# Kernel optimization log

Hardware: AMD Instinct MI355X
Metric: run time of the kernel (lower is better)

Reference implementation:

```python
import jax, jax.numpy as jnp
import numpy as np

OUT, IN = 8192, 8192
GROUP = 128
N_GROUPS = IN // GROUP
BATCH = 64


def dequant_int4(packed, scales):
    # packed: [OUT, IN//2] int32 bytes in [0,256); two 4-bit codes per byte
    low = packed & 0xF            # first element of each pair
    high = (packed >> 4) & 0xF    # second element
    q = jnp.stack([low, high], axis=-1).reshape(OUT, IN)  # interleaved nibbles
    # symmetric grouped dequant: w = (q - 8) * scale, scale per [row, group]
    qg = q.reshape(OUT, N_GROUPS, GROUP).astype(scales.dtype)
    w = (qg - 8.0) * scales[:, :, None]
    return w.reshape(OUT, IN)


def setup_inputs() -> dict:
    key = jax.random.key(0)
    k1, k2, k3 = jax.random.split(key, 3)
    x = jax.random.normal(k1, (BATCH, IN), dtype=jnp.float32)
    packed = jax.random.randint(k2, (OUT, IN // 2), 0, 256, dtype=jnp.int32)
    scales = jax.random.uniform(k3, (OUT, N_GROUPS), dtype=jnp.float32)
    return {"x": x, "packed": packed, "scales": scales}


def reference(x, packed, scales):
    # Dequantize int4 weights then dense matmul (F.linear, no bias)
    w = dequant_int4(packed, scales)        # [OUT, IN]
    return jnp.einsum('bi,oi->bo', x, w)    # [BATCH, OUT]
```

## Files before the change

kernel.cpp:

```cpp
#include <hip/hip_runtime.h>
#include <hip/hip_bf16.h>
#include <stdint.h>

#define OUTN   8192
#define INN    8192
#define NGRP   64
#define BATCHN 64
#define KSPLIT 8
#define KCHUNK (INN / KSPLIT)
#define NITER  (KCHUNK / 128)
#define OSZ    (BATCHN * OUTN)

typedef __attribute__((ext_vector_type(8))) short bf16x8;
typedef __attribute__((ext_vector_type(4))) float f32x4;
typedef __attribute__((ext_vector_type(4))) unsigned int u32x4;

__device__ __forceinline__ unsigned short f2bf(float f) {
  __hip_bfloat16 h = __float2bfloat16(f);
  return __builtin_bit_cast(unsigned short, h);
}
__device__ __forceinline__ float bf2f(unsigned short h) {
  unsigned int u = ((unsigned int)h) << 16;
  return __builtin_bit_cast(float, u);
}

__global__ void qlin_prep(const float* __restrict__ x, float* __restrict__ xsum) {
  const int b = blockIdx.x;
  const int t = threadIdx.x;
  const float* xrow = x + (size_t)b * INN + t * 32;
  float s = 0.0f;
#pragma unroll
  for (int i = 0; i < 8; ++i) {
    float4 v = *(const float4*)(xrow + i * 4);
    s += bf2f(f2bf(v.x)) + bf2f(f2bf(v.y)) + bf2f(f2bf(v.z)) + bf2f(f2bf(v.w));
  }
  __shared__ float part[256];
  part[t] = s;
  __syncthreads();
  if (t < NGRP) {
    float g = part[4 * t] + part[4 * t + 1] + part[4 * t + 2] + part[4 * t + 3];
    xsum[t * BATCHN + b] = g;
  }
}

__global__ void qlin_swz(const float* __restrict__ x, unsigned short* __restrict__ xswz) {
  const int idx = blockIdx.x * 256 + threadIdx.x;
  const int b  = idx & 63;
  const int kb = idx >> 6;
  const float* p = x + (size_t)b * INN + kb * 8;
  float4 v0 = *(const float4*)p;
  float4 v1 = *(const float4*)(p + 4);
  u32x4 o;
  o.x = (unsigned)f2bf(v0.x) | ((unsigned)f2bf(v0.y) << 16);
  o.y = (unsigned)f2bf(v0.z) | ((unsigned)f2bf(v0.w) << 16);
  o.z = (unsigned)f2bf(v1.x) | ((unsigned)f2bf(v1.y) << 16);
  o.w = (unsigned)f2bf(v1.z) | ((unsigned)f2bf(v1.w) << 16);
  *(u32x4*)&xswz[(size_t)idx * 8] = o;
}

__global__ __launch_bounds__(256, 4) void qlin_main(
    const int* __restrict__ packed, const float* __restrict__ scales,
    const unsigned short* __restrict__ xswz, const float* __restrict__ xsum,
    float* __restrict__ out, float* __restrict__ part) {
  const int bx    = blockIdx.x;
  const int ks    = bx & (KSPLIT - 1);
  const int ntile = bx >> 3;
  const int o0    = ntile * 64;
  const int g0    = ks * NITER;

  const int t    = threadIdx.x;
  const int lane = t & 63;
  const int w    = t >> 6;
  const int r    = lane & 15;
  const int q    = lane >> 4;
  const int orow = o0 + w * 16 + r;

  __shared__ float xs[NITER][BATCHN];
#pragma unroll
  for (int i = 0; i < 2; ++i) {
    int v = t * 2 + i;
    xs[v >> 6][v & 63] = xsum[(g0 + (v >> 6)) * BATCHN + (v & 63)];
  }

  float4 sa = *(const float4*)&scales[(size_t)orow * NGRP + g0];
  float4 sb = *(const float4*)&scales[(size_t)orow * NGRP + g0 + 4];
  float sreg[8] = {sa.x, sa.y, sa.z, sa.w, sb.x, sb.y, sb.z, sb.w};

  const int* bptr = packed + (size_t)orow * (INN / 2) + ks * (KCHUNK / 2) + q * 4;
  const unsigned short* aptr = xswz + ((size_t)(ks * 128 + q) * 64 + r) * 8;

  __syncthreads();

  f32x4 facc[4];
#pragma unroll
  for (int mt = 0; mt < 4; ++mt) facc[mt] = (f32x4){0.f, 0.f, 0.f, 0.f};

  int4 b4[4], b4n[4];
#pragma unroll
  for (int kq = 0; kq < 4; ++kq) b4[kq] = *(const int4*)(bptr + kq * 16);

  for (int i = 0; i < NITER; ++i) {
    f32x4 gacc[4];
#pragma unroll
    for (int mt = 0; mt < 4; ++mt) gacc[mt] = (f32x4){0.f, 0.f, 0.f, 0.f};

#pragma unroll
    for (int kq = 0; kq < 4; ++kq) {
      bf16x8 af[4];
#pragma unroll
      for (int mt = 0; mt < 4; ++mt)
        af[mt] = *(const bf16x8*)(aptr + ((size_t)(i * 16 + kq * 4) * 64 + mt * 16) * 8);

      int4 c = b4[kq];
      u32x4 bw0, bw1;
      bw0.x = 0x43004300u | ((unsigned)c.x & 0xFu) | (((unsigned)c.x & 0xF0u) << 12);
      bw0.y = 0x43004300u | ((unsigned)c.y & 0xFu) | (((unsigned)c.y & 0xF0u) << 12);
      bw0.z = 0x43004300u | ((unsigned)c.z & 0xFu) | (((unsigned)c.z & 0xF0u) << 12);
      bw0.w = 0x43004300u | ((unsigned)c.w & 0xFu) | (((unsigned)c.w & 0xF0u) << 12);
      bf16x8 bfv;
      bfv[0] = (short)(bw0.x & 0xFFFF); bfv[1] = (short)(bw0.x >> 16);
      bfv[2] = (short)(bw0.y & 0xFFFF); bfv[3] = (short)(bw0.y >> 16);
      bfv[4] = (short)(bw0.z & 0xFFFF); bfv[5] = (short)(bw0.z >> 16);
      bfv[6] = (short)(bw0.w & 0xFFFF); bfv[7] = (short)(bw0.w >> 16);
      (void)bw1;

#pragma unroll
      for (int mt = 0; mt < 4; ++mt)
        gacc[mt] = __builtin_amdgcn_mfma_f32_16x16x32_bf16(af[mt], bfv, gacc[mt], 0, 0, 0);
    }

    if (i + 1 < NITER) {
#pragma unroll
      for (int kq = 0; kq < 4; ++kq)
        b4n[kq] = *(const int4*)(bptr + (i + 1) * 64 + kq * 16);
    }

    float s0 = sreg[i];
#pragma unroll
    for (int mt = 0; mt < 4; ++mt) {
      f32x4 xv = *(const f32x4*)&xs[i][mt * 16 + q * 4];
#pragma unroll
      for (int rr = 0; rr < 4; ++rr)
        facc[mt][rr] += s0 * (gacc[mt][rr] - 136.0f * xv[rr]);
    }

#pragma unroll
    for (int kq = 0; kq < 4; ++kq) b4[kq] = b4n[kq];
  }

  if (part) {
    float* pb = part + (size_t)ks * OSZ;
#pragma unroll
    for (int mt = 0; mt < 4; ++mt)
#pragma unroll
      for (int rr = 0; rr < 4; ++rr) {
        int m = mt * 16 + q * 4 + rr;
        pb[(size_t)m * OUTN + orow] = facc[mt][rr];
      }
  } else {
#pragma unroll
    for (int mt = 0; mt < 4; ++mt)
#pragma unroll
      for (int rr = 0; rr < 4; ++rr) {
        int m = mt * 16 + q * 4 + rr;
        atomicAdd(&out[(size_t)m * OUTN + orow], facc[mt][rr]);
      }
  }
}

__global__ void qlin_reduce(const float* __restrict__ part, float* __restrict__ out) {
  const size_t i = ((size_t)blockIdx.x * 256 + threadIdx.x) * 4;
  float4 s = *(const float4*)(part + i);
#pragma unroll
  for (int ks = 1; ks < KSPLIT; ++ks) {
    float4 v = *(const float4*)(part + (size_t)ks * OSZ + i);
    s.x += v.x; s.y += v.y; s.z += v.z; s.w += v.w;
  }
  *(float4*)(out + i) = s;
}

extern "C" void kernel_launch(void* const* d_in, const int* in_sizes, int n_in,
                              void* d_out, int out_size, void* d_ws, size_t ws_size,
                              hipStream_t stream) {
  const float* x      = (const float*)d_in[0];
  const int*   packed = (const int*)d_in[1];
  const float* scales = (const float*)d_in[2];
  float* out = (float*)d_out;

  char* ws = (char*)d_ws;
  float*          xsum = (float*)ws;
  unsigned short* xswz = (unsigned short*)(ws + 16384);
  const size_t part_need = 16384 + 1048576 + (size_t)KSPLIT * OSZ * sizeof(float);
  float* part = (ws_size >= part_need) ? (float*)(ws + 16384 + 1048576) : nullptr;

  qlin_prep<<<BATCHN, 256, 0, stream>>>(x, xsum);
  qlin_swz<<<(INN / 8) * BATCHN / 256, 256, 0, stream>>>(x, xswz);
  if (!part)
    hipMemsetAsync(d_out, 0, (size_t)out_size * sizeof(float), stream);
  qlin_main<<<(OUTN / 64) * KSPLIT, 256, 0, stream>>>(packed, scales, xswz, xsum, out, part);
  if (part)
    qlin_reduce<<<OSZ / 4 / 256, 256, 0, stream>>>(part, out);
}
```

Baseline: 217.5 us.

## Deepen register prefetch pipeline for weights and activations in main loop

Replaces the single-stage weight prefetch with a three-deep register ring for packed weights and a two-deep ring for activation fragments, fully unrolling the group loop so loads for group g+2 are issued while MFMAs for group g run. Dequant is factored into a helper that bit-casts instead of assembling the vector element by element. Launch bounds drop from 4 to 2 waves per SIMD to leave room for the larger register footprint. This aims to hide global-load latency, at the cost of lower occupancy and higher register pressure.

```diff
diff --git a/kernel.cpp b/kernel.cpp
--- a/kernel.cpp
+++ b/kernel.cpp
@@ -58,7 +58,16 @@
   *(u32x4*)&xswz[(size_t)idx * 8] = o;
 }
 
-__global__ __launch_bounds__(256, 4) void qlin_main(
+__device__ __forceinline__ bf16x8 dequant8(int4 c) {
+  u32x4 bw;
+  bw.x = 0x43004300u | ((unsigned)c.x & 0xFu) | (((unsigned)c.x & 0xF0u) << 12);
+  bw.y = 0x43004300u | ((unsigned)c.y & 0xFu) | (((unsigned)c.y & 0xF0u) << 12);
+  bw.z = 0x43004300u | ((unsigned)c.z & 0xFu) | (((unsigned)c.z & 0xF0u) << 12);
+  bw.w = 0x43004300u | ((unsigned)c.w & 0xFu) | (((unsigned)c.w & 0xF0u) << 12);
+  return __builtin_bit_cast(bf16x8, bw);
+}
+
+__global__ __launch_bounds__(256, 2) void qlin_main(
     const int* __restrict__ packed, const float* __restrict__ scales,
     const unsigned short* __restrict__ xswz, const float* __restrict__ xsum,
     float* __restrict__ out, float* __restrict__ part) {
@@ -81,6 +90,7 @@
     int v = t * 2 + i;
     xs[v >> 6][v & 63] = xsum[(g0 + (v >> 6)) * BATCHN + (v & 63)];
   }
+  __syncthreads();
 
   float4 sa = *(const float4*)&scales[(size_t)orow * NGRP + g0];
   float4 sb = *(const float4*)&scales[(size_t)orow * NGRP + g0 + 4];
@@ -89,63 +99,56 @@
   const int* bptr = packed + (size_t)orow * (INN / 2) + ks * (KCHUNK / 2) + q * 4;
   const unsigned short* aptr = xswz + ((size_t)(ks * 128 + q) * 64 + r) * 8;
 
-  __syncthreads();
+  int4  bv[3][4];
+  u32x4 av[2][16];
+
+  auto loadB = [&](int g, int4* dst) {
+#pragma unroll
+    for (int s = 0; s < 4; ++s)
+      dst[s] = *(const int4*)(bptr + g * 64 + s * 16);
+  };
+  auto loadA = [&](int g, u32x4* dst) {
+#pragma unroll
+    for (int s = 0; s < 4; ++s)
+#pragma unroll
+      for (int mt = 0; mt < 4; ++mt)
+        dst[s * 4 + mt] = *(const u32x4*)(aptr + ((size_t)(g * 16 + s * 4) * 64 + mt * 16) * 8);
+  };
+
+  loadB(0, bv[0]); loadB(1, bv[1]);
+  loadA(0, av[0]); loadA(1, av[1]);
 
   f32x4 facc[4];
 #pragma unroll
   for (int mt = 0; mt < 4; ++mt) facc[mt] = (f32x4){0.f, 0.f, 0.f, 0.f};
 
-  int4 b4[4], b4n[4];
-#pragma unroll
-  for (int kq = 0; kq < 4; ++kq) b4[kq] = *(const int4*)(bptr + kq * 16);
-
-  for (int i = 0; i < NITER; ++i) {
+#pragma unroll
+  for (int g = 0; g < NITER; ++g) {
+    if (g + 2 < NITER) loadB(g + 2, bv[(g + 2) % 3]);
+
     f32x4 gacc[4];
 #pragma unroll
     for (int mt = 0; mt < 4; ++mt) gacc[mt] = (f32x4){0.f, 0.f, 0.f, 0.f};
 
 #pragma unroll
-    for (int kq = 0; kq < 4; ++kq) {
-      bf16x8 af[4];
+    for (int s = 0; s < 4; ++s) {
+      bf16x8 bfv = dequant8(bv[g % 3][s]);
 #pragma unroll
       for (int mt = 0; mt < 4; ++mt)
-        af[mt] = *(const bf16x8*)(aptr + ((size_t)(i * 16 + kq * 4) * 64 + mt * 16) * 8);
-
-      int4 c = b4[kq];
-      u32x4 bw0, bw1;
-      bw0.x = 0x43004300u | ((unsigned)c.x & 0xFu) | (((unsigned)c.x & 0xF0u) << 12);
-      bw0.y = 0x43004300u | ((unsigned)c.y & 0xFu) | (((unsigned)c.y & 0xF0u) << 12);
-      bw0.z = 0x43004300u | ((unsigned)c.z & 0xFu) | (((unsigned)c.z & 0xF0u) << 12);
-      bw0.w = 0x43004300u | ((unsigned)c.w & 0xFu) | (((unsigned)c.w & 0xF0u) << 12);
-      bf16x8 bfv;
-      bfv[0] = (short)(bw0.x & 0xFFFF); bfv[1] = (short)(bw0.x >> 16);
-      bfv[2] = (short)(bw0.y & 0xFFFF); bfv[3] = (short)(bw0.y >> 16);
-      bfv[4] = (short)(bw0.z & 0xFFFF); bfv[5] = (short)(bw0.z >> 16);
-      bfv[6] = (short)(bw0.w & 0xFFFF); bfv[7] = (short)(bw0.w >> 16);
-      (void)bw1;
-
-#pragma unroll
-      for (int mt = 0; mt < 4; ++mt)
-        gacc[mt] = __builtin_amdgcn_mfma_f32_16x16x32_bf16(af[mt], bfv, gacc[mt], 0, 0, 0);
+        gacc[mt] = __builtin_amdgcn_mfma_f32_16x16x32_bf16(
+            __builtin_bit_cast(bf16x8, av[g & 1][s * 4 + mt]), bfv, gacc[mt], 0, 0, 0);
     }
 
-    if (i + 1 < NITER) {
-#pragma unroll
-      for (int kq = 0; kq < 4; ++kq)
-        b4n[kq] = *(const int4*)(bptr + (i + 1) * 64 + kq * 16);
+    if (g + 2 < NITER) loadA(g + 2, av[g & 1]);
+
+    float sg = sreg[g];
+#pragma unroll
+    for (int mt = 0; mt < 4; ++mt) {
+      f32x4 xv = *(const f32x4*)&xs[g][mt * 16 + q * 4];
+#pragma unroll
+      for (int rr = 0; rr < 4; ++rr)
+        facc[mt][rr] += sg * (gacc[mt][rr] - 136.0f * xv[rr]);
     }
-
-    float s0 = sreg[i];
-#pragma unroll
-    for (int mt = 0; mt < 4; ++mt) {
-      f32x4 xv = *(const f32x4*)&xs[i][mt * 16 + q * 4];
-#pragma unroll
-      for (int rr = 0; rr < 4; ++rr)
-        facc[mt][rr] += s0 * (gacc[mt][rr] - 136.0f * xv[rr]);
-    }
-
-#pragma unroll
-    for (int kq = 0; kq < 4; ++kq) b4[kq] = b4n[kq];
   }
 
   if (part) {
```

Result: no change. 221.9 us (+2.0%).

## Stage packed weights and activations through LDS with register-prefetched double loop

Applied to the files above, without the earlier changes.

The main kernel now loads tiles of packed weights and bf16 activations cooperatively into registers, compacts each group of four int32 bytes into one 32-bit word, and stores both into padded shared memory. MFMA operands are then read from shared memory. Activations are rewritten in plain row-major bf16 instead of the MFMA-swizzled layout. The intent is coalesced global loads, and activation fragments shared by all waves instead of each wave fetching them from global memory. The cost is two barriers per iteration and extra LDS traffic, which could reduce occupancy.

```diff
diff --git a/kernel.cpp b/kernel.cpp
--- a/kernel.cpp
+++ b/kernel.cpp
@@ -6,14 +6,18 @@
 #define INN    8192
 #define NGRP   64
 #define BATCHN 64
+#define BN     64
+#define BK     128
 #define KSPLIT 8
 #define KCHUNK (INN / KSPLIT)
-#define NITER  (KCHUNK / 128)
+#define NITER  (KCHUNK / BK)
 #define OSZ    (BATCHN * OUTN)
 
 typedef __attribute__((ext_vector_type(8))) short bf16x8;
 typedef __attribute__((ext_vector_type(4))) float f32x4;
 typedef __attribute__((ext_vector_type(4))) unsigned int u32x4;
+
+#define BARRIER_KEEP_VMEM() asm volatile("s_waitcnt lgkmcnt(0)\n\ts_barrier" ::: "memory")
 
 __device__ __forceinline__ unsigned short f2bf(float f) {
   __hip_bfloat16 h = __float2bfloat16(f);
@@ -45,9 +49,9 @@
 
 __global__ void qlin_swz(const float* __restrict__ x, unsigned short* __restrict__ xswz) {
   const int idx = blockIdx.x * 256 + threadIdx.x;
-  const int b  = idx & 63;
-  const int kb = idx >> 6;
-  const float* p = x + (size_t)b * INN + kb * 8;
+  const int b  = idx >> 10;
+  const int kc = idx & 1023;
+  const float* p = x + (size_t)b * INN + kc * 8;
   float4 v0 = *(const float4*)p;
   float4 v1 = *(const float4*)(p + 4);
   u32x4 o;
@@ -55,8 +59,11 @@
   o.y = (unsigned)f2bf(v0.z) | ((unsigned)f2bf(v0.w) << 16);
   o.z = (unsigned)f2bf(v1.x) | ((unsigned)f2bf(v1.y) << 16);
   o.w = (unsigned)f2bf(v1.z) | ((unsigned)f2bf(v1.w) << 16);
-  *(u32x4*)&xswz[(size_t)idx * 8] = o;
-}
+  *(u32x4*)&xswz[(size_t)b * INN + kc * 8] = o;
+}
+
+#define PKS 17
+#define XTS 136
 
 __global__ __launch_bounds__(256, 4) void qlin_main(
     const int* __restrict__ packed, const float* __restrict__ scales,
@@ -65,7 +72,7 @@
   const int bx    = blockIdx.x;
   const int ks    = bx & (KSPLIT - 1);
   const int ntile = bx >> 3;
-  const int o0    = ntile * 64;
+  const int o0    = ntile * BN;
   const int g0    = ks * NITER;
 
   const int t    = threadIdx.x;
@@ -75,7 +82,10 @@
   const int q    = lane >> 4;
   const int orow = o0 + w * 16 + r;
 
-  __shared__ float xs[NITER][BATCHN];
+  __shared__ __align__(16) unsigned int   pk_c[BN * PKS];
+  __shared__ __align__(16) unsigned short xt[BATCHN * XTS];
+  __shared__ __align__(16) float          xs[NITER][BATCHN];
+
 #pragma unroll
   for (int i = 0; i < 2; ++i) {
     int v = t * 2 + i;
@@ -86,20 +96,48 @@
   float4 sb = *(const float4*)&scales[(size_t)orow * NGRP + g0 + 4];
   float sreg[8] = {sa.x, sa.y, sa.z, sa.w, sb.x, sb.y, sb.z, sb.w};
 
-  const int* bptr = packed + (size_t)orow * (INN / 2) + ks * (KCHUNK / 2) + q * 4;
-  const unsigned short* aptr = xswz + ((size_t)(ks * 128 + q) * 64 + r) * 8;
-
-  __syncthreads();
+  int4  pkr[4];
+  u32x4 xr4[4];
+  const int prow = t >> 4, pcol = t & 15;
+  const int xrow = t >> 2, xseg = t & 3;
+
+  auto load_tile = [&](int i) {
+    const int kk2 = ks * (KCHUNK / 2) + i * (BK / 2);
+    const int* pbase = packed + (size_t)(o0 + prow) * (INN / 2) + kk2 + pcol * 4;
+#pragma unroll
+    for (int j = 0; j < 4; ++j)
+      pkr[j] = *(const int4*)(pbase + (size_t)(16 * j) * (INN / 2));
+    const unsigned short* xbase =
+        xswz + (size_t)xrow * INN + ks * KCHUNK + i * BK + xseg * 32;
+#pragma unroll
+    for (int j = 0; j < 4; ++j)
+      xr4[j] = *(const u32x4*)(xbase + j * 8);
+  };
+
+  auto store_tile = [&]() {
+#pragma unroll
+    for (int j = 0; j < 4; ++j) {
+      unsigned int c = (unsigned)pkr[j].x | ((unsigned)pkr[j].y << 8) |
+                       ((unsigned)pkr[j].z << 16) | ((unsigned)pkr[j].w << 24);
+      pk_c[(prow + 16 * j) * PKS + pcol] = c;
+    }
+#pragma unroll
+    for (int j = 0; j < 4; ++j)
+      *(u32x4*)&xt[xrow * XTS + xseg * 32 + j * 8] = xr4[j];
+  };
 
   f32x4 facc[4];
 #pragma unroll
   for (int mt = 0; mt < 4; ++mt) facc[mt] = (f32x4){0.f, 0.f, 0.f, 0.f};
 
-  int4 b4[4], b4n[4];
-#pragma unroll
-  for (int kq = 0; kq < 4; ++kq) b4[kq] = *(const int4*)(bptr + kq * 16);
+  load_tile(0);
 
   for (int i = 0; i < NITER; ++i) {
+    BARRIER_KEEP_VMEM();
+    store_tile();
+    if (i + 1 < NITER) load_tile(i + 1);
+    BARRIER_KEEP_VMEM();
+
     f32x4 gacc[4];
 #pragma unroll
     for (int mt = 0; mt < 4; ++mt) gacc[mt] = (f32x4){0.f, 0.f, 0.f, 0.f};
@@ -109,43 +147,29 @@
       bf16x8 af[4];
 #pragma unroll
       for (int mt = 0; mt < 4; ++mt)
-        af[mt] = *(const bf16x8*)(aptr + ((size_t)(i * 16 + kq * 4) * 64 + mt * 16) * 8);
-
-      int4 c = b4[kq];
-      u32x4 bw0, bw1;
-      bw0.x = 0x43004300u | ((unsigned)c.x & 0xFu) | (((unsigned)c.x & 0xF0u) << 12);
-      bw0.y = 0x43004300u | ((unsigned)c.y & 0xFu) | (((unsigned)c.y & 0xF0u) << 12);
-      bw0.z = 0x43004300u | ((unsigned)c.z & 0xFu) | (((unsigned)c.z & 0xF0u) << 12);
-      bw0.w = 0x43004300u | ((unsigned)c.w & 0xFu) | (((unsigned)c.w & 0xF0u) << 12);
-      bf16x8 bfv;
-      bfv[0] = (short)(bw0.x & 0xFFFF); bfv[1] = (short)(bw0.x >> 16);
-      bfv[2] = (short)(bw0.y & 0xFFFF); bfv[3] = (short)(bw0.y >> 16);
-      bfv[4] = (short)(bw0.z & 0xFFFF); bfv[5] = (short)(bw0.z >> 16);
-      bfv[6] = (short)(bw0.w & 0xFFFF); bfv[7] = (short)(bw0.w >> 16);
-      (void)bw1;
+        af[mt] = *(const bf16x8*)&xt[(mt * 16 + r) * XTS + kq * 32 + q * 8];
+
+      unsigned int c = pk_c[(w * 16 + r) * PKS + kq * 4 + q];
+      u32x4 bw;
+      bw.x = 0x43004300u | (c & 0xFu) | ((c & 0xF0u) << 12);
+      bw.y = 0x43004300u | ((c >> 8) & 0xFu) | (((c >> 8) & 0xF0u) << 12);
+      bw.z = 0x43004300u | ((c >> 16) & 0xFu) | (((c >> 16) & 0xF0u) << 12);
+      bw.w = 0x43004300u | ((c >> 24) & 0xFu) | (((c >> 24) & 0xF0u) << 12);
+      bf16x8 bfv = __builtin_bit_cast(bf16x8, bw);
 
 #pragma unroll
       for (int mt = 0; mt < 4; ++mt)
         gacc[mt] = __builtin_amdgcn_mfma_f32_16x16x32_bf16(af[mt], bfv, gacc[mt], 0, 0, 0);
     }
 
-    if (i + 1 < NITER) {
-#pragma unroll
-      for (int kq = 0; kq < 4; ++kq)
-        b4n[kq] = *(const int4*)(bptr + (i + 1) * 64 + kq * 16);
-    }
-
-    float s0 = sreg[i];
+    float sg = sreg[i];
 #pragma unroll
     for (int mt = 0; mt < 4; ++mt) {
       f32x4 xv = *(const f32x4*)&xs[i][mt * 16 + q * 4];
 #pragma unroll
       for (int rr = 0; rr < 4; ++rr)
-        facc[mt][rr] += s0 * (gacc[mt][rr] - 136.0f * xv[rr]);
+        facc[mt][rr] += sg * (gacc[mt][rr] - 136.0f * xv[rr]);
     }
-
-#pragma unroll
-    for (int kq = 0; kq < 4; ++kq) b4[kq] = b4n[kq];
   }
 
   if (part) {
@@ -194,10 +218,10 @@
   float* part = (ws_size >= part_need) ? (float*)(ws + 16384 + 1048576) : nullptr;
 
   qlin_prep<<<BATCHN, 256, 0, stream>>>(x, xsum);
-  qlin_swz<<<(INN / 8) * BATCHN / 256, 256, 0, stream>>>(x, xswz);
+  qlin_swz<<<(BATCHN * INN / 8) / 256, 256, 0, stream>>>(x, xswz);
   if (!part)
     hipMemsetAsync(d_out, 0, (size_t)out_size * sizeof(float), stream);
-  qlin_main<<<(OUTN / 64) * KSPLIT, 256, 0, stream>>>(packed, scales, xswz, xsum, out, part);
+  qlin_main<<<(OUTN / BN) * KSPLIT, 256, 0, stream>>>(packed, scales, xswz, xsum, out, part);
   if (part)
     qlin_reduce<<<OSZ / 4 / 256, 256, 0, stream>>>(part, out);
 }
```

Result: faster. 209.3 us (-3.8%).
